# Kernel optimization log

Hardware: AMD Instinct MI355X
Metric: run time of the kernel (lower is better)

## Reference

```python
import jax, jax.numpy as jnp
import numpy as np

N_NODES = 100000
N_EDGES = 3200000
IN_DIM = 512
HID_DIM = 16


def spmm(edge_src, edge_dst, edge_weight, feats):
    # out[i] = sum_{(j->i) in E} w_e * feats[j]  (sparse adj @ feats)
    gathered = feats[edge_src] * edge_weight[:, None]  # [E, D]
    return jax.ops.segment_sum(gathered, edge_dst, num_segments=N_NODES)


def setup_inputs() -> dict:
    key = jax.random.key(0)
    ks = jax.random.split(key, 8)
    x = jax.random.normal(ks[0], (N_NODES, IN_DIM), dtype=jnp.float32)
    edge_src = jax.random.randint(ks[1], (N_EDGES,), 0, N_NODES, dtype=jnp.int32)
    edge_dst = jax.random.randint(ks[2], (N_EDGES,), 0, N_NODES, dtype=jnp.int32)
    # normalized adjacency weights (positive, small, like D^-1/2 A D^-1/2 entries)
    edge_weight = jax.random.uniform(ks[3], (N_EDGES,), dtype=jnp.float32) * 0.1
    # Glorot-style init for GraphConvolution weights
    W1 = jax.random.normal(ks[4], (IN_DIM, HID_DIM), dtype=jnp.float32) * (1.0 / np.sqrt(IN_DIM))
    b1 = jnp.zeros((HID_DIM,), dtype=jnp.float32)
    W2 = jax.random.normal(ks[5], (HID_DIM, 1), dtype=jnp.float32) * (1.0 / np.sqrt(HID_DIM))
    b2 = jnp.zeros((1,), dtype=jnp.float32)
    return {"x": x, "edge_src": edge_src, "edge_dst": edge_dst,
            "edge_weight": edge_weight, "W1": W1, "b1": b1, "W2": W2, "b2": b2}


def reference(x, edge_src, edge_dst, edge_weight, W1, b1, W2, b2):
    # Layer 1: GraphConvolution(input_dim -> hidden_dim) + ReLU
    h = spmm(edge_src, edge_dst, edge_weight, x @ W1) + b1  # [N, 16]
    h = jax.nn.relu(h)
    # dropout is identity in eval mode (training=False)
    # Layer 2: GraphConvolution(hidden_dim -> 1)
    out = spmm(edge_src, edge_dst, edge_weight, h @ W2) + b2  # [N, 1]
    return out
```

## Files before the change

### kernel.cpp

```cpp
#include <hip/hip_runtime.h>
#include <hip/hip_fp16.h>

#define N_NODES 100000
#define N_EDGES 3200000
#define IN_DIM  512
#define HID_DIM 16

#define B_BKT   782
#define BKT_SH  7
#define EPB     12500
#define CAP_MAX 4608

#define G1_TILES 6250

typedef __attribute__((ext_vector_type(8))) short bf16x8;
typedef __attribute__((ext_vector_type(4))) float f32x4;

__device__ __forceinline__ void atomic_add_f32(float* p, float v) {
    __hip_atomic_fetch_add(p, v, __ATOMIC_RELAXED, __HIP_MEMORY_SCOPE_AGENT);
}
__device__ __forceinline__ int atomic_add_i32(int* p, int v) {
    return __hip_atomic_fetch_add(p, v, __ATOMIC_RELAXED, __HIP_MEMORY_SCOPE_AGENT);
}

__device__ __forceinline__ unsigned short bf16_rne(float f) {
    unsigned u = __float_as_uint(f);
    return (unsigned short)((u + 0x7fffu + ((u >> 16) & 1u)) >> 16);
}

__global__ void z0_init(int* __restrict__ cursor, int cap) {
    int b = blockIdx.x * blockDim.x + threadIdx.x;
    if (b < B_BKT) cursor[b] = b * cap;
}

__global__ __launch_bounds__(256) void g1_xw_mfma(const float* __restrict__ x,
                                                  const float* __restrict__ W1,
                                                  __half* __restrict__ xwh) {
    __shared__ alignas(16) unsigned short whi[16 * 64 * 8];
    __shared__ alignas(16) unsigned short wlo[16 * 64 * 8];
    const int t = threadIdx.x;

    for (int idx = t; idx < 16 * 64 * 8; idx += 256) {
        int c  = idx >> 9;
        int l  = (idx >> 3) & 63;
        int tt = idx & 7;
        int k  = c * 32 + ((l >> 4) << 3) + tt;
        int j  = l & 15;
        float w = W1[k * HID_DIM + j];
        unsigned u = __float_as_uint(w);
        float hif = __uint_as_float(u & 0xffff0000u);
        whi[idx] = (unsigned short)(u >> 16);
        wlo[idx] = bf16_rne(w - hif);
    }
    __syncthreads();

    const int lane = t & 63;
    const int wid  = blockIdx.x * 4 + (t >> 6);
    if (wid >= G1_TILES) return;
    const int row0 = wid * 16;

    const float* xrow = x + (size_t)(row0 + (lane & 15)) * IN_DIM + ((lane >> 4) << 3);
    const unsigned short* whp = &whi[lane * 8];
    const unsigned short* wlp = &wlo[lane * 8];

    f32x4 acc = {0.f, 0.f, 0.f, 0.f};
    float4 p0[2], p1[2];
    p0[0] = *(const float4*)(xrow);
    p1[0] = *(const float4*)(xrow + 4);
    p0[1] = *(const float4*)(xrow + 32);
    p1[1] = *(const float4*)(xrow + 36);
#pragma unroll
    for (int c = 0; c < 16; ++c) {
        const int cur = c & 1;
        float4 n0, n1;
        if (c < 14) {
            n0 = *(const float4*)(xrow + (c + 2) * 32);
            n1 = *(const float4*)(xrow + (c + 2) * 32 + 4);
        }
        float av[8] = {p0[cur].x, p0[cur].y, p0[cur].z, p0[cur].w,
                       p1[cur].x, p1[cur].y, p1[cur].z, p1[cur].w};
        bf16x8 ah, al;
#pragma unroll
        for (int e = 0; e < 8; ++e) {
            unsigned u = __float_as_uint(av[e]);
            ah[e] = (short)(u >> 16);
            float lof = av[e] - __uint_as_float(u & 0xffff0000u);
            al[e] = (short)bf16_rne(lof);
        }
        bf16x8 bh = *(const bf16x8*)(whp + (size_t)c * 512);
        bf16x8 bl = *(const bf16x8*)(wlp + (size_t)c * 512);
        acc = __builtin_amdgcn_mfma_f32_16x16x32_bf16(ah, bh, acc, 0, 0, 0);
        acc = __builtin_amdgcn_mfma_f32_16x16x32_bf16(al, bh, acc, 0, 0, 0);
        acc = __builtin_amdgcn_mfma_f32_16x16x32_bf16(ah, bl, acc, 0, 0, 0);
        if (c < 14) { p0[cur] = n0; p1[cur] = n1; }
    }

    const int n     = lane & 15;
    const int rbase = row0 + ((lane >> 4) << 2);
#pragma unroll
    for (int i = 0; i < 4; ++i)
        xwh[(size_t)(rbase + i) * HID_DIM + n] = __float2half_rn(acc[i]);
}

__global__ __launch_bounds__(1024) void s1_bin(const int* __restrict__ src,
                                               const int* __restrict__ dst,
                                               const float* __restrict__ wgt,
                                               int* __restrict__ cursor,
                                               uint2* __restrict__ rec, int cap) {
    __shared__ int hist[B_BKT];
    __shared__ int base[B_BKT];
    const int t = threadIdx.x;
    for (int b = t; b < B_BKT; b += 1024) hist[b] = 0;
    __syncthreads();
    const int e0 = blockIdx.x * EPB;
    const int4*   d4 = (const int4*)(dst + e0);
    const int4*   s4 = (const int4*)(src + e0);
    const float4* w4 = (const float4*)(wgt + e0);
    const int NG = EPB / 4;
    for (int g = t; g < NG; g += 1024) {
        int4 d = d4[g];
        atomicAdd(&hist[d.x >> BKT_SH], 1);
        atomicAdd(&hist[d.y >> BKT_SH], 1);
        atomicAdd(&hist[d.z >> BKT_SH], 1);
        atomicAdd(&hist[d.w >> BKT_SH], 1);
    }
    __syncthreads();
    for (int b = t; b < B_BKT; b += 1024) {
        int c = hist[b];
        base[b] = c > 0 ? atomic_add_i32(&cursor[b], c) : 0;
    }
    __syncthreads();
    for (int b = t; b < B_BKT; b += 1024) hist[b] = 0;
    __syncthreads();
    for (int g = t; g < NG; g += 1024) {
        int4 d = d4[g];
        int4 s = s4[g];
        float4 w = w4[g];
        {
            int b = d.x >> BKT_SH;
            int pos = base[b] + atomicAdd(&hist[b], 1);
            rec[pos] = make_uint2(((unsigned)s.x << BKT_SH) | (unsigned)(d.x & 127),
                                  __float_as_uint(w.x));
        }
        {
            int b = d.y >> BKT_SH;
            int pos = base[b] + atomicAdd(&hist[b], 1);
            rec[pos] = make_uint2(((unsigned)s.y << BKT_SH) | (unsigned)(d.y & 127),
                                  __float_as_uint(w.y));
        }
        {
            int b = d.z >> BKT_SH;
            int pos = base[b] + atomicAdd(&hist[b], 1);
            rec[pos] = make_uint2(((unsigned)s.z << BKT_SH) | (unsigned)(d.z & 127),
                                  __float_as_uint(w.z));
        }
        {
            int b = d.w >> BKT_SH;
            int pos = base[b] + atomicAdd(&hist[b], 1);
            rec[pos] = make_uint2(((unsigned)s.w << BKT_SH) | (unsigned)(d.w & 127),
                                  __float_as_uint(w.w));
        }
    }
}

__global__ __launch_bounds__(512) void s2_sort(const int* __restrict__ cursor,
                                               uint2* __restrict__ rec,
                                               int2* __restrict__ row, int cap) {
    __shared__ uint2 srec[CAP_MAX];
    __shared__ int ocnt[128], scn[128], cur[128];
    const int t = threadIdx.x;
    const int bkt = blockIdx.x;
    const int e0 = bkt * cap;
    int n = cursor[bkt] - e0;
    n = max(0, min(n, cap));
    if (t < 128) ocnt[t] = 0;
    __syncthreads();
    for (int i = t; i < n; i += 512) {
        uint2 r = rec[e0 + i];
        srec[i] = r;
        atomicAdd(&ocnt[r.x & 127u], 1);
    }
    __syncthreads();
    if (t < 128) scn[t] = ocnt[t];
    __syncthreads();
    for (int off = 1; off < 128; off <<= 1) {
        int v = 0;
        if (t < 128 && t >= off) v = scn[t - off];
        __syncthreads();
        if (t < 128 && t >= off) scn[t] += v;
        __syncthreads();
    }
    if (t < 128) {
        int b = scn[t] - ocnt[t];
        cur[t] = b;
        int node = (bkt << BKT_SH) + t;
        if (node < N_NODES) row[node] = make_int2(e0 + b, ocnt[t]);
    }
    __syncthreads();
    for (int i = t; i < n; i += 512) {
        uint2 r = srec[i];
        int d = (int)(r.x & 127u);
        int pos = atomicAdd(&cur[d], 1);
        rec[e0 + pos] = make_uint2(r.x >> BKT_SH, r.y);
    }
}

__global__ __launch_bounds__(256) void p4_layer1(const int2* __restrict__ row,
                                                 const uint2* __restrict__ rec,
                                                 const __half* __restrict__ xwh,
                                                 const float* __restrict__ b1,
                                                 const float* __restrict__ W2,
                                                 float* __restrict__ hw) {
    const int t = threadIdx.x;
    const int node = blockIdx.x * 16 + (t >> 4);
    const int j = t & 15;
    int2 r = row[node];
    int e = r.x;
    const int end = r.x + r.y;
    float acc = 0.0f;
    for (; e + 4 <= end; e += 4) {
        uint2 q0 = rec[e], q1 = rec[e + 1], q2 = rec[e + 2], q3 = rec[e + 3];
        float f0 = __half2float(xwh[(size_t)q0.x * HID_DIM + j]);
        float f1 = __half2float(xwh[(size_t)q1.x * HID_DIM + j]);
        float f2 = __half2float(xwh[(size_t)q2.x * HID_DIM + j]);
        float f3 = __half2float(xwh[(size_t)q3.x * HID_DIM + j]);
        acc += __uint_as_float(q0.y) * f0;
        acc += __uint_as_float(q1.y) * f1;
        acc += __uint_as_float(q2.y) * f2;
        acc += __uint_as_float(q3.y) * f3;
    }
    for (; e < end; ++e) {
        uint2 q = rec[e];
        acc += __uint_as_float(q.y) * __half2float(xwh[(size_t)q.x * HID_DIM + j]);
    }
    float v = fmaxf(acc + b1[j], 0.0f) * W2[j];
    v += __shfl_xor(v, 1);
    v += __shfl_xor(v, 2);
    v += __shfl_xor(v, 4);
    v += __shfl_xor(v, 8);
    if (j == 0) hw[node] = v;
}

__global__ __launch_bounds__(256) void p5_layer2(const int2* __restrict__ row,
                                                 const uint2* __restrict__ rec,
                                                 const float* __restrict__ hwv,
                                                 const float* __restrict__ b2,
                                                 float* __restrict__ out) {
    const int t = threadIdx.x;
    const int node = blockIdx.x * 32 + (t >> 3);
    const int i = t & 7;
    int2 r = row[node];
    const int end = r.x + r.y;
    int k = r.x + i;
    float s = 0.0f;
    for (; k + 24 < end; k += 32) {
        uint2 a = rec[k], b = rec[k + 8], c = rec[k + 16], d = rec[k + 24];
        float ha = hwv[a.x], hb = hwv[b.x], hc = hwv[c.x], hd = hwv[d.x];
        s += __uint_as_float(a.y) * ha + __uint_as_float(b.y) * hb
           + __uint_as_float(c.y) * hc + __uint_as_float(d.y) * hd;
    }
    for (; k < end; k += 8) {
        uint2 a = rec[k];
        s += __uint_as_float(a.y) * hwv[a.x];
    }
    s += __shfl_xor(s, 1);
    s += __shfl_xor(s, 2);
    s += __shfl_xor(s, 4);
    if (i == 0) out[node] = b2[0] + s;
}

__global__ void f0_zero(float* __restrict__ h, const float* __restrict__ b2,
                        float* __restrict__ out) {
    int i = blockIdx.x * blockDim.x + threadIdx.x;
    if (i < N_NODES * HID_DIM) h[i] = 0.0f;
    if (i < N_NODES) out[i] = b2[0];
}
__global__ void k2_spmm1(const int* __restrict__ src, const int* __restrict__ dst,
                         const float* __restrict__ wgt, const __half* __restrict__ xwh,
                         float* __restrict__ h) {
    int t = blockIdx.x * blockDim.x + threadIdx.x;
    int e = t >> 4;
    int j = t & (HID_DIM - 1);
    if (e < N_EDGES) {
        float v = wgt[e] * __half2float(xwh[(size_t)src[e] * HID_DIM + j]);
        atomic_add_f32(&h[(size_t)dst[e] * HID_DIM + j], v);
    }
}
__global__ void k3_act(const float* __restrict__ h, const float* __restrict__ b1,
                       const float* __restrict__ W2, float* __restrict__ hw) {
    int i = blockIdx.x * blockDim.x + threadIdx.x;
    if (i >= N_NODES) return;
    const float4* h4 = (const float4*)(h + (size_t)i * HID_DIM);
    const float4* b4 = (const float4*)b1;
    const float4* w4 = (const float4*)W2;
    float acc = 0.0f;
#pragma unroll
    for (int q = 0; q < HID_DIM / 4; ++q) {
        float4 hv = h4[q]; float4 bv = b4[q]; float4 wv = w4[q];
        acc += fmaxf(hv.x + bv.x, 0.0f) * wv.x;
        acc += fmaxf(hv.y + bv.y, 0.0f) * wv.y;
        acc += fmaxf(hv.z + bv.z, 0.0f) * wv.z;
        acc += fmaxf(hv.w + bv.w, 0.0f) * wv.w;
    }
    hw[i] = acc;
}
__global__ void k4_spmm2(const int* __restrict__ src, const int* __restrict__ dst,
                         const float* __restrict__ wgt, const float* __restrict__ hw,
                         float* __restrict__ out) {
    int e = blockIdx.x * blockDim.x + threadIdx.x;
    if (e < N_EDGES) atomic_add_f32(&out[dst[e]], wgt[e] * hw[src[e]]);
}


extern "C" void kernel_launch(void* const* d_in, const int* in_sizes, int n_in,
                              void* d_out, int out_size, void* d_ws, size_t ws_size,
                              hipStream_t stream) {
    const float* x    = (const float*)d_in[0];
    const int*   esrc = (const int*)  d_in[1];
    const int*   edst = (const int*)  d_in[2];
    const float* ew   = (const float*)d_in[3];
    const float* W1   = (const float*)d_in[4];
    const float* b1   = (const float*)d_in[5];
    const float* W2   = (const float*)d_in[6];
    const float* b2   = (const float*)d_in[7];
    float* out = (float*)d_out;
    char* ws = (char*)d_ws;

    __half* xwh    = (__half*)ws;
    float*  hw     = (float*)(ws + (size_t)N_NODES * HID_DIM * 2);
    int*    cursor = (int*)(hw + N_NODES);
    int2*   row    = (int2*)(((size_t)(cursor + B_BKT) + 7) & ~(size_t)7);
    size_t rec_off = ((size_t)((char*)(row + N_NODES) - ws) + 15) & ~(size_t)15;
    uint2* rec = (uint2*)(ws + rec_off);

    int cap = 0;
    if (ws_size > rec_off) {
        size_t cap_fit = (ws_size - rec_off) / ((size_t)B_BKT * sizeof(uint2));
        cap = (int)(cap_fit < CAP_MAX ? cap_fit : CAP_MAX);
    }

    if (cap >= 4480) {
        z0_init<<<(B_BKT + 255) / 256, 256, 0, stream>>>(cursor, cap);
        g1_xw_mfma<<<(G1_TILES + 3) / 4, 256, 0, stream>>>(x, W1, xwh);
        s1_bin<<<N_EDGES / EPB, 1024, 0, stream>>>(esrc, edst, ew, cursor, rec, cap);
        s2_sort<<<B_BKT, 512, 0, stream>>>(cursor, rec, row, cap);
        p4_layer1<<<N_NODES / 16, 256, 0, stream>>>(row, rec, xwh, b1, W2, hw);
        p5_layer2<<<N_NODES / 32, 256, 0, stream>>>(row, rec, hw, b2, out);
    } else {
        __half* f_xwh = (__half*)ws;
        float*  f_h   = (float*)(ws + (size_t)N_NODES * HID_DIM * 2);
        float*  f_hw  = f_h + (size_t)N_NODES * HID_DIM;
        int n = N_NODES * HID_DIM;
        f0_zero<<<(n + 255) / 256, 256, 0, stream>>>(f_h, b2, out);
        g1_xw_mfma<<<(G1_TILES + 3) / 4, 256, 0, stream>>>(x, W1, f_xwh);
        k2_spmm1<<<(N_EDGES * 16) / 256, 256, 0, stream>>>(esrc, edst, ew, f_xwh, f_h);
        k3_act<<<(N_NODES + 255) / 256, 256, 0, stream>>>(f_h, b1, W2, f_hw);
        k4_spmm2<<<(N_EDGES + 255) / 256, 256, 0, stream>>>(esrc, edst, ew, f_hw, out);
    }
}
```

Baseline: 443.2 us.

## Fuse bucket sort with layer-1 aggregation using LDS-resident sorted edges

Merges the per-bucket counting sort and the layer-1 SpMM into one kernel. After scattering records into shared memory by destination, the block writes them back to global for layer 2, then computes each node's hidden activation straight from the LDS copy. This drops one kernel launch and a full global re-read of the sorted edge records. The cost is that layer-1 work now runs on only 782 blocks of 512 threads instead of 6250 small blocks, and each block reads its bucket from global twice.

New measurement: 418.4 us. 1.06x faster.

```diff
diff --git a/kernel.cpp b/kernel.cpp
--- a/kernel.cpp
+++ b/kernel.cpp
@@ -163,10 +163,14 @@
     }
 }
 
-__global__ __launch_bounds__(512) void s2_sort(const int* __restrict__ cursor,
-                                               uint2* __restrict__ rec,
-                                               int2* __restrict__ row, int cap) {
-    __shared__ uint2 srec[CAP_MAX];
+__global__ __launch_bounds__(512) void s2p4(const int* __restrict__ cursor,
+                                            uint2* __restrict__ rec,
+                                            int2* __restrict__ row,
+                                            const __half* __restrict__ xwh,
+                                            const float* __restrict__ b1,
+                                            const float* __restrict__ W2,
+                                            float* __restrict__ hw, int cap) {
+    __shared__ uint2 srt[CAP_MAX];
     __shared__ int ocnt[128], scn[128], cur[128];
     const int t = threadIdx.x;
     const int bkt = blockIdx.x;
@@ -175,11 +179,8 @@
     n = max(0, min(n, cap));
     if (t < 128) ocnt[t] = 0;
     __syncthreads();
-    for (int i = t; i < n; i += 512) {
-        uint2 r = rec[e0 + i];
-        srec[i] = r;
-        atomicAdd(&ocnt[r.x & 127u], 1);
-    }
+    for (int i = t; i < n; i += 512)
+        atomicAdd(&ocnt[rec[e0 + i].x & 127u], 1);
     __syncthreads();
     if (t < 128) scn[t] = ocnt[t];
     __syncthreads();
@@ -198,47 +199,42 @@
     }
     __syncthreads();
     for (int i = t; i < n; i += 512) {
-        uint2 r = srec[i];
+        uint2 r = rec[e0 + i];
         int d = (int)(r.x & 127u);
         int pos = atomicAdd(&cur[d], 1);
-        rec[e0 + pos] = make_uint2(r.x >> BKT_SH, r.y);
-    }
-}
-
-__global__ __launch_bounds__(256) void p4_layer1(const int2* __restrict__ row,
-                                                 const uint2* __restrict__ rec,
-                                                 const __half* __restrict__ xwh,
-                                                 const float* __restrict__ b1,
-                                                 const float* __restrict__ W2,
-                                                 float* __restrict__ hw) {
-    const int t = threadIdx.x;
-    const int node = blockIdx.x * 16 + (t >> 4);
+        srt[pos] = make_uint2(r.x >> BKT_SH, r.y);
+    }
+    __syncthreads();
+    for (int i = t; i < n; i += 512) rec[e0 + i] = srt[i];
     const int j = t & 15;
-    int2 r = row[node];
-    int e = r.x;
-    const int end = r.x + r.y;
-    float acc = 0.0f;
-    for (; e + 4 <= end; e += 4) {
-        uint2 q0 = rec[e], q1 = rec[e + 1], q2 = rec[e + 2], q3 = rec[e + 3];
-        float f0 = __half2float(xwh[(size_t)q0.x * HID_DIM + j]);
-        float f1 = __half2float(xwh[(size_t)q1.x * HID_DIM + j]);
-        float f2 = __half2float(xwh[(size_t)q2.x * HID_DIM + j]);
-        float f3 = __half2float(xwh[(size_t)q3.x * HID_DIM + j]);
-        acc += __uint_as_float(q0.y) * f0;
-        acc += __uint_as_float(q1.y) * f1;
-        acc += __uint_as_float(q2.y) * f2;
-        acc += __uint_as_float(q3.y) * f3;
-    }
-    for (; e < end; ++e) {
-        uint2 q = rec[e];
-        acc += __uint_as_float(q.y) * __half2float(xwh[(size_t)q.x * HID_DIM + j]);
-    }
-    float v = fmaxf(acc + b1[j], 0.0f) * W2[j];
-    v += __shfl_xor(v, 1);
-    v += __shfl_xor(v, 2);
-    v += __shfl_xor(v, 4);
-    v += __shfl_xor(v, 8);
-    if (j == 0) hw[node] = v;
+    for (int g = (t >> 4); g < 128; g += 32) {
+        const int node = (bkt << BKT_SH) + g;
+        if (node >= N_NODES) continue;
+        int e = scn[g] - ocnt[g];
+        const int end = scn[g];
+        float acc = 0.0f;
+        for (; e + 4 <= end; e += 4) {
+            uint2 q0 = srt[e], q1 = srt[e + 1], q2 = srt[e + 2], q3 = srt[e + 3];
+            float f0 = __half2float(xwh[(size_t)q0.x * HID_DIM + j]);
+            float f1 = __half2float(xwh[(size_t)q1.x * HID_DIM + j]);
+            float f2 = __half2float(xwh[(size_t)q2.x * HID_DIM + j]);
+            float f3 = __half2float(xwh[(size_t)q3.x * HID_DIM + j]);
+            acc += __uint_as_float(q0.y) * f0;
+            acc += __uint_as_float(q1.y) * f1;
+            acc += __uint_as_float(q2.y) * f2;
+            acc += __uint_as_float(q3.y) * f3;
+        }
+        for (; e < end; ++e) {
+            uint2 q = srt[e];
+            acc += __uint_as_float(q.y) * __half2float(xwh[(size_t)q.x * HID_DIM + j]);
+        }
+        float v = fmaxf(acc + b1[j], 0.0f) * W2[j];
+        v += __shfl_xor(v, 1);
+        v += __shfl_xor(v, 2);
+        v += __shfl_xor(v, 4);
+        v += __shfl_xor(v, 8);
+        if (j == 0) hw[node] = v;
+    }
 }
 
 __global__ __launch_bounds__(256) void p5_layer2(const int2* __restrict__ row,
@@ -343,8 +339,7 @@
         z0_init<<<(B_BKT + 255) / 256, 256, 0, stream>>>(cursor, cap);
         g1_xw_mfma<<<(G1_TILES + 3) / 4, 256, 0, stream>>>(x, W1, xwh);
         s1_bin<<<N_EDGES / EPB, 1024, 0, stream>>>(esrc, edst, ew, cursor, rec, cap);
-        s2_sort<<<B_BKT, 512, 0, stream>>>(cursor, rec, row, cap);
-        p4_layer1<<<N_NODES / 16, 256, 0, stream>>>(row, rec, xwh, b1, W2, hw);
+        s2p4<<<B_BKT, 512, 0, stream>>>(cursor, rec, row, xwh, b1, W2, hw, cap);
         p5_layer2<<<N_NODES / 32, 256, 0, stream>>>(row, rec, hw, b2, out);
     } else {
         __half* f_xwh = (__half*)ws;
```
